# Kernel tuning notes

Measured on AMD Instinct MI355X. Metric: run time of the kernel, lower is better.

Reference implementation:

```python
import jax, jax.numpy as jnp
import numpy as np

# Structural constants (derived from anchors_list in the original forward)
NUM_PER_LEVEL = [98304, 49152, 24576, 12288, 6144]
NUM_ANCHORS_PER_LOC = 3
CAND_PER_LEVEL = 9  # candidate_number_of_positive_anchors_per_level
SMOOTH_L1_NA = 3.0  # self.num_anchors -> smooth-L1 beta = 1/3
INF = 100000000.0


def _build_anchors():
    parts = []
    for lvl, n in enumerate(NUM_PER_LEVEL):
        locs = n // NUM_ANCHORS_PER_LOC
        stride = 8.0 * (2 ** lvl)
        centers = (np.arange(locs) + 0.5) * stride
        base = 16.0 * (2 ** lvl)
        widths = base * np.array([1.0, 2 ** (1.0 / 3.0), 2 ** (2.0 / 3.0)])
        c = np.repeat(centers, NUM_ANCHORS_PER_LOC)
        w = np.tile(widths, locs)
        parts.append(np.stack([c - w / 2.0, c + w / 2.0], axis=1))
    return np.concatenate(parts, axis=0).astype(np.float32)


def setup_inputs() -> dict:
    key = jax.random.key(0)
    k1, k2, k3 = jax.random.split(key, 3)
    anchors = jnp.asarray(_build_anchors())  # [A, 2]
    A = anchors.shape[0]
    B, M = 4, 64
    extent = (NUM_PER_LEVEL[0] // NUM_ANCHORS_PER_LOC) * 8.0
    centers = jax.random.uniform(k1, (B, M), minval=0.0, maxval=extent)
    widths = jax.random.uniform(k2, (B, M), minval=50.0, maxval=500.0)
    # class column = 0, class_id = 1 -> every GT row survives the filter
    annotations = jnp.stack(
        [centers - widths / 2.0, centers + widths / 2.0, jnp.zeros((B, M))], axis=-1
    ).astype(jnp.float32)
    regressions = jax.random.normal(k3, (B, A, 2), dtype=jnp.float32)
    return {"regressions": regressions, "anchors": anchors,
            "annotations": annotations, "class_id": 1}


def _calc_iou_1d(a, b):
    # a: [A,2] anchors, b: [M,2] gt intervals -> IoU [A, M]
    inter = jnp.clip(
        jnp.minimum(a[:, 1][:, None], b[:, 1][None, :])
        - jnp.maximum(a[:, 0][:, None], b[:, 0][None, :]), 0.0)
    union = (a[:, 1] - a[:, 0])[:, None] + (b[:, 1] - b[:, 0])[None, :] - inter
    return inter / jnp.clip(union, 1e-8)


def _atss_l1_loss_single(regression, annotation, anchors):
    A = anchors.shape[0]
    M = annotation.shape[0]
    iou = _calc_iou_1d(anchors, annotation[:, :2])  # [A, M]

    anchor_cx = (anchors[:, 0] + anchors[:, 1]) / 2.0
    gt_cx = (annotation[:, 0] + annotation[:, 1]) / 2.0
    # gt_y and anchor_y are both 0 -> Euclidean distance reduces to |dx|
    dist = jnp.abs(anchor_cx[:, None] - gt_cx[None, :])  # [A, M]

    # per-level topk (smallest distance) candidates
    cand_idx_list = []
    start = 0
    for n in NUM_PER_LEVEL:
        topk = min(CAND_PER_LEVEL * NUM_ANCHORS_PER_LOC, n)
        _, idx = jax.lax.top_k(-dist[start:start + n].T, topk)  # [M, topk]
        cand_idx_list.append(idx.T + start)
        start += n
    cand_idx = jnp.concatenate(cand_idx_list, axis=0)  # [K, M], K = 27*levels
    K = cand_idx.shape[0]

    cand_iou = jnp.take_along_axis(iou, cand_idx, axis=0)  # [K, M]
    iou_mean = cand_iou.mean(axis=0)
    iou_std = jnp.sqrt(jnp.sum((cand_iou - iou_mean[None, :]) ** 2, axis=0)
                       / (K - 1))  # unbiased, like torch.std
    thresh = iou_mean + iou_std
    is_pos = cand_iou >= thresh[None, :]

    # candidate center must be inside the gt interval (margin 0.01)
    cand_cx = anchor_cx[cand_idx]  # [K, M]
    l = cand_cx - annotation[None, :, 0]
    r = annotation[None, :, 1] - cand_cx
    is_pos = is_pos & (jnp.minimum(l, r) > 0.01)

    # scatter candidate IoUs into [M*A] buffer of -INF, then per-anchor argmax over gts
    flat_idx = (cand_idx + jnp.arange(M)[None, :] * A).ravel()  # unique indices
    iou_t_flat = iou.T.ravel()
    vals = jnp.where(is_pos.ravel(), iou_t_flat[flat_idx], -INF)
    ious_inf = jnp.full((M * A,), -INF, dtype=iou.dtype).at[flat_idx].set(vals)
    ious_inf = ious_inf.reshape(M, A).T  # [A, M]

    best_val = ious_inf.max(axis=1)
    best_idx = jnp.argmax(ious_inf, axis=1)
    pos = best_val != -INF  # [A]

    assigned = annotation[best_idx]  # [A, 3]
    anchor_w = anchors[:, 1] - anchors[:, 0]
    anchor_c = anchors[:, 0] + 0.5 * anchor_w
    gt_w_raw = assigned[:, 1] - assigned[:, 0]
    gt_c = assigned[:, 0] + 0.5 * gt_w_raw  # center uses unclamped width
    gt_w = jnp.clip(gt_w_raw, 1.0)

    dx = (gt_c - anchor_c) / anchor_w / 0.1
    dw = jnp.log(gt_w / anchor_w) / 0.2
    targets = jnp.stack([dx, dw], axis=-1)  # [A, 2]

    diff = jnp.abs(targets - regression)
    beta = 1.0 / SMOOTH_L1_NA
    loss = jnp.where(diff <= beta,
                     0.5 * SMOOTH_L1_NA * diff ** 2,
                     diff - 0.5 / SMOOTH_L1_NA)
    mask = pos.astype(loss.dtype)[:, None]
    num_pos = jnp.sum(pos)
    loss_mean = jnp.sum(loss * mask) / jnp.maximum(num_pos * 2, 1).astype(loss.dtype)
    return jnp.where(num_pos > 0, loss_mean, jnp.zeros((), loss.dtype))


def reference(regressions, anchors, annotations, class_id):
    # class_id only drives the GT filter; inputs are built so all rows are kept
    # (class column != -1 and != class_id).
    per_image = jax.vmap(lambda r, a: _atss_l1_loss_single(r, a, anchors))
    return per_image(regressions, annotations)  # [B] per-image losses
```

## Files before the change

### kernel.cpp

```cpp
#include <hip/hip_runtime.h>


static constexpr int NLEV = 5;
static constexpr int B_IMG = 4;
static constexpr int M_GT = 64;
static constexpr int A_TOTAL = 190464;
static constexpr int K_CAND = 135;
static constexpr int BM_TOTAL = B_IMG * M_GT;
static constexpr int REC_STRIDE = 136;
static constexpr int SLICES = 16;
static constexpr int MAX_J = 9;
static constexpr unsigned long long PACK_BIAS = 0xB000000000000000ULL;

__device__ __constant__ int d_LOCS[NLEV]   = {32768, 16384, 8192, 4096, 2048};
__device__ __constant__ int d_ASTART[NLEV] = {0, 98304, 147456, 172032, 184320};

__global__ __launch_bounds__(64) void atss_assign(
    const float* __restrict__ reg,
    const float* __restrict__ anchors,
    const float* __restrict__ ann,
    unsigned long long* __restrict__ packed,
    unsigned long long* __restrict__ rec)
{
    const int bm = blockIdx.x;
    const int b = bm >> 6;
    const int m = bm & 63;
    const int lane = threadIdx.x;

    const float g0 = ann[(b * M_GT + m) * 3 + 0];
    const float g1 = ann[(b * M_GT + m) * 3 + 1];
    const float gcx = (g0 + g1) * 0.5f;

    int   j_[NLEV];
    float a0v[NLEV], a1v[NLEV];
#pragma unroll
    for (int lvl = 0; lvl < NLEV; ++lvl) {
        const int locs = d_LOCS[lvl];
        const int base = d_ASTART[lvl];
        const float stride = (float)(8 << lvl);
        int j = (int)(gcx / stride);
        if (j < 0) j = 0;
        if (j > locs - 1) j = locs - 1;
        j_[lvl] = j;
        const int t = j - 10 + lane;
        const bool v = (lane < 21) && (t >= 0) && (t < locs);
        const int a = base + 3 * t;
        a0v[lvl] = v ? anchors[2 * a]     : 0.0f;
        a1v[lvl] = v ? anchors[2 * a + 1] : 0.0f;
    }

    int winStart[NLEV];
#pragma unroll
    for (int lvl = 0; lvl < NLEV; ++lvl) {
        const int locs = d_LOCS[lvl];
        const int j = j_[lvl];
        const int t = j - 10 + lane;
        const bool v = (lane < 21) && (t >= 0) && (t < locs);
        const float dist =
            v ? fabsf((a0v[lvl] + a1v[lvl]) * 0.5f - gcx) : INFINITY;

        int bi = 10;
        float bd = INFINITY;
#pragma unroll
        for (int li = 9; li <= 11; ++li) {
            const float d = __shfl(dist, li);
            if (d < bd) { bd = d; bi = li; }
        }

        int lo = bi, hi = bi;
#pragma unroll
        for (int s = 0; s < 8; ++s) {
            const float dl = __shfl(dist, lo - 1);
            const float dr = __shfl(dist, hi + 1);
            if (dl <= dr) --lo; else ++hi;
        }
        winStart[lvl] = (j - 10) + lo;
    }

    float ci[3];
    int   ca[3];
    bool  cok[3];
    float ca0[3], ca1[3];
#pragma unroll
    for (int i = 0; i < 3; ++i) {
        const int k = lane + 64 * i;
        ci[i] = 0.0f; ca[i] = -1; cok[i] = false; ca0[i] = 0.0f; ca1[i] = 1.0f;
        if (k < K_CAND) {
            const int lvl = k / 27;
            const int r = k % 27;
            const int loc = winStart[lvl] + r / 3;
            const int a = d_ASTART[lvl] + loc * 3 + (r % 3);
            const float a0 = anchors[2 * a];
            const float a1 = anchors[2 * a + 1];
            float inter = fminf(a1, g1) - fmaxf(a0, g0);
            inter = fmaxf(inter, 0.0f);
            const float uni = (a1 - a0) + (g1 - g0) - inter;
            const float iou = inter / fmaxf(uni, 1e-8f);
            const float cx = (a0 + a1) * 0.5f;
            ci[i] = iou;
            ca[i] = a;
            ca0[i] = a0;
            ca1[i] = a1;
            cok[i] = fminf(cx - g0, g1 - cx) > 0.01f;
        }
    }

    float r0[3], r1[3];
#pragma unroll
    for (int i = 0; i < 3; ++i) {
        r0[i] = 0.0f; r1[i] = 0.0f;
        if (ca[i] >= 0) {
            const float* r = reg + ((size_t)b * A_TOTAL + ca[i]) * 2;
            r0[i] = r[0];
            r1[i] = r[1];
        }
    }

    float s = ci[0] + ci[1] + ci[2];
#pragma unroll
    for (int off = 32; off >= 1; off >>= 1) s += __shfl_xor(s, off);
    const float mean = s / 135.0f;

    float s2 = 0.0f;
#pragma unroll
    for (int i = 0; i < 3; ++i) {
        if (ca[i] >= 0) { const float d = ci[i] - mean; s2 += d * d; }
    }
#pragma unroll
    for (int off = 32; off >= 1; off >>= 1) s2 += __shfl_xor(s2, off);
    const float thresh = mean + sqrtf(s2 / 134.0f);

    unsigned long long* pb = packed + (size_t)b * A_TOTAL;
    bool pos[3];
#pragma unroll
    for (int i = 0; i < 3; ++i) {
        pos[i] = (ca[i] >= 0) && cok[i] && (ci[i] >= thresh);
        if (pos[i]) {
            const unsigned long long pk =
                (((unsigned long long)__float_as_uint(ci[i]) << 32) |
                 (unsigned int)(~m)) + PACK_BIAS;
            atomicMax(pb + ca[i], pk);
        }
    }

    const float gwr = g1 - g0;
    const float gc = g0 + 0.5f * gwr;
    const float gw = fmaxf(gwr, 1.0f);
    float lossv[3];
#pragma unroll
    for (int i = 0; i < 3; ++i) {
        lossv[i] = 0.0f;
        if (pos[i]) {
            const float a0 = ca0[i];
            const float a1 = ca1[i];
            const float aw = a1 - a0;
            const float acx = a0 + 0.5f * aw;
            const float dx = (gc - acx) / aw / 0.1f;
            const float dw = logf(gw / aw) / 0.2f;
            const float d0 = fabsf(dx - r0[i]);
            const float d1 = fabsf(dw - r1[i]);
            const float beta = 1.0f / 3.0f;
            const float l0 = (d0 <= beta) ? 0.5f * 3.0f * d0 * d0 : d0 - 0.5f / 3.0f;
            const float l1 = (d1 <= beta) ? 0.5f * 3.0f * d1 * d1 : d1 - 0.5f / 3.0f;
            lossv[i] = l0 + l1;
        }
    }

    const unsigned long long m0 = __ballot(pos[0]);
    const unsigned long long m1 = __ballot(pos[1]);
    const unsigned long long m2 = __ballot(pos[2]);
    const int c0 = __popcll(m0);
    const int c1 = __popcll(m1);
    const unsigned long long below63 =
        (lane == 63) ? 0x7FFFFFFFFFFFFFFFULL : ((1ULL << lane) - 1ULL);
    const int base = bm * REC_STRIDE;
    int offs[3];
    offs[0] = __popcll(m0 & below63);
    offs[1] = c0 + __popcll(m1 & below63);
    offs[2] = c0 + c1 + __popcll(m2 & below63);
#pragma unroll
    for (int i = 0; i < 3; ++i) {
        if (pos[i]) {
            rec[base + offs[i]] =
                ((unsigned long long)__float_as_uint(lossv[i]) << 32) |
                ((unsigned long long)(unsigned int)m << 18) |
                (unsigned int)ca[i];
        }
    }
    if (lane == 0) {
        rec[base + (REC_STRIDE - 1)] =
            (unsigned long long)(c0 + c1 + __popcll(m2));
    }
}

__global__ __launch_bounds__(1024) void atss_resolve(
    const unsigned long long* __restrict__ packed,
    const unsigned long long* __restrict__ rec,
    float* __restrict__ out)
{
    const int b = blockIdx.x;
    const int tid = threadIdx.x;
    const int gt = tid >> 4;
    const int slice = tid & 15;
    const int wave = tid >> 6;
    const int lane = tid & 63;

    const int region = b * M_GT + gt;
    const int base = region * REC_STRIDE;
    const unsigned long long* pb = packed + (size_t)b * A_TOTAL;

    const unsigned long long cv = rec[base + (REC_STRIDE - 1)];
    unsigned long long al[MAX_J];
#pragma unroll
    for (int j = 0; j < MAX_J; ++j) {
        al[j] = rec[base + slice + SLICES * j];
    }

    unsigned int c = (unsigned int)cv;
    if (c > (unsigned int)K_CAND) c = K_CAND;

    unsigned long long cur[MAX_J];
#pragma unroll
    for (int j = 0; j < MAX_J; ++j) {
        const bool valid = (unsigned int)(slice + SLICES * j) < c;
        const unsigned int a = (unsigned int)al[j] & 0x3FFFFu;
        cur[j] = valid
            ? __hip_atomic_load(pb + a, __ATOMIC_RELAXED,
                                __HIP_MEMORY_SCOPE_AGENT)
            : 0ULL;
    }

    float L = 0.0f, C = 0.0f;
#pragma unroll
    for (int j = 0; j < MAX_J; ++j) {
        if ((unsigned int)(slice + SLICES * j) < c) {
            const unsigned int mr = ((unsigned int)al[j] >> 18) & 63u;
            if ((unsigned int)cur[j] == ~mr) {
                L += __uint_as_float((unsigned int)(al[j] >> 32));
                C += 1.0f;
            }
        }
    }

#pragma unroll
    for (int off = 32; off >= 1; off >>= 1) {
        L += __shfl_xor(L, off);
        C += __shfl_xor(C, off);
    }

    __shared__ float sl[16];
    __shared__ float sc[16];
    if (lane == 0) { sl[wave] = L; sc[wave] = C; }
    __syncthreads();

    if (tid == 0) {
        float Lt = 0.0f, Ct = 0.0f;
#pragma unroll
        for (int w = 0; w < 16; ++w) { Lt += sl[w]; Ct += sc[w]; }
        const unsigned int np = (unsigned int)Ct;
        const unsigned int denom = (2u * np > 1u) ? 2u * np : 1u;
        out[b] = (np > 0) ? Lt / (float)denom : 0.0f;
    }
}

extern "C" void kernel_launch(void* const* d_in, const int* in_sizes, int n_in,
                              void* d_out, int out_size, void* d_ws, size_t ws_size,
                              hipStream_t stream) {
    const float* reg     = (const float*)d_in[0];
    const float* anchors = (const float*)d_in[1];
    const float* ann     = (const float*)d_in[2];
    float* out = (float*)d_out;

    char* p = (char*)d_ws;
    unsigned long long* packed = (unsigned long long*)p;
    p += (size_t)B_IMG * A_TOTAL * 8;
    unsigned long long* rec = (unsigned long long*)p;

    atss_assign<<<BM_TOTAL, 64, 0, stream>>>(reg, anchors, ann, packed, rec);
    atss_resolve<<<B_IMG, 1024, 0, stream>>>(packed, rec, out);
}
```

Baseline: 15.53 us.

## Fuse assign and resolve kernels into one launch with flag-based inter-block sync

Merges the per-GT assignment kernel and the per-image resolve kernel into a single launch. Sixteen producer blocks of 16 waves each replace the 256 single-wave blocks, and publish their records with agent-scope atomic stores plus a release flag per GT. Four consumer blocks spin on those flags with sleep before reading. This removes the second kernel launch and its dependency gap. In exchange it relies on all blocks being co-resident, and on the flag region not holding magic values left over from an earlier call.

```diff
diff --git a/kernel.cpp b/kernel.cpp
--- a/kernel.cpp
+++ b/kernel.cpp
@@ -10,196 +10,214 @@
 static constexpr int REC_STRIDE = 136;
 static constexpr int SLICES = 16;
 static constexpr int MAX_J = 9;
+static constexpr int PROD_BLOCKS = 16;
 static constexpr unsigned long long PACK_BIAS = 0xB000000000000000ULL;
+static constexpr unsigned long long FLAG_MAGIC = 0x5AFEC0DEF00D0000ULL;
 
 __device__ __constant__ int d_LOCS[NLEV]   = {32768, 16384, 8192, 4096, 2048};
 __device__ __constant__ int d_ASTART[NLEV] = {0, 98304, 147456, 172032, 184320};
 
-__global__ __launch_bounds__(64) void atss_assign(
+__global__ __launch_bounds__(1024) void atss_fused(
     const float* __restrict__ reg,
     const float* __restrict__ anchors,
     const float* __restrict__ ann,
     unsigned long long* __restrict__ packed,
-    unsigned long long* __restrict__ rec)
-{
-    const int bm = blockIdx.x;
-    const int b = bm >> 6;
-    const int m = bm & 63;
-    const int lane = threadIdx.x;
-
-    const float g0 = ann[(b * M_GT + m) * 3 + 0];
-    const float g1 = ann[(b * M_GT + m) * 3 + 1];
-    const float gcx = (g0 + g1) * 0.5f;
-
-    int   j_[NLEV];
-    float a0v[NLEV], a1v[NLEV];
-#pragma unroll
-    for (int lvl = 0; lvl < NLEV; ++lvl) {
-        const int locs = d_LOCS[lvl];
-        const int base = d_ASTART[lvl];
-        const float stride = (float)(8 << lvl);
-        int j = (int)(gcx / stride);
-        if (j < 0) j = 0;
-        if (j > locs - 1) j = locs - 1;
-        j_[lvl] = j;
-        const int t = j - 10 + lane;
-        const bool v = (lane < 21) && (t >= 0) && (t < locs);
-        const int a = base + 3 * t;
-        a0v[lvl] = v ? anchors[2 * a]     : 0.0f;
-        a1v[lvl] = v ? anchors[2 * a + 1] : 0.0f;
-    }
-
-    int winStart[NLEV];
-#pragma unroll
-    for (int lvl = 0; lvl < NLEV; ++lvl) {
-        const int locs = d_LOCS[lvl];
-        const int j = j_[lvl];
-        const int t = j - 10 + lane;
-        const bool v = (lane < 21) && (t >= 0) && (t < locs);
-        const float dist =
-            v ? fabsf((a0v[lvl] + a1v[lvl]) * 0.5f - gcx) : INFINITY;
-
-        int bi = 10;
-        float bd = INFINITY;
-#pragma unroll
-        for (int li = 9; li <= 11; ++li) {
-            const float d = __shfl(dist, li);
-            if (d < bd) { bd = d; bi = li; }
-        }
-
-        int lo = bi, hi = bi;
-#pragma unroll
-        for (int s = 0; s < 8; ++s) {
-            const float dl = __shfl(dist, lo - 1);
-            const float dr = __shfl(dist, hi + 1);
-            if (dl <= dr) --lo; else ++hi;
-        }
-        winStart[lvl] = (j - 10) + lo;
-    }
-
-    float ci[3];
-    int   ca[3];
-    bool  cok[3];
-    float ca0[3], ca1[3];
-#pragma unroll
-    for (int i = 0; i < 3; ++i) {
-        const int k = lane + 64 * i;
-        ci[i] = 0.0f; ca[i] = -1; cok[i] = false; ca0[i] = 0.0f; ca1[i] = 1.0f;
-        if (k < K_CAND) {
-            const int lvl = k / 27;
-            const int r = k % 27;
-            const int loc = winStart[lvl] + r / 3;
-            const int a = d_ASTART[lvl] + loc * 3 + (r % 3);
-            const float a0 = anchors[2 * a];
-            const float a1 = anchors[2 * a + 1];
-            float inter = fminf(a1, g1) - fmaxf(a0, g0);
-            inter = fmaxf(inter, 0.0f);
-            const float uni = (a1 - a0) + (g1 - g0) - inter;
-            const float iou = inter / fmaxf(uni, 1e-8f);
-            const float cx = (a0 + a1) * 0.5f;
-            ci[i] = iou;
-            ca[i] = a;
-            ca0[i] = a0;
-            ca1[i] = a1;
-            cok[i] = fminf(cx - g0, g1 - cx) > 0.01f;
-        }
-    }
-
-    float r0[3], r1[3];
-#pragma unroll
-    for (int i = 0; i < 3; ++i) {
-        r0[i] = 0.0f; r1[i] = 0.0f;
-        if (ca[i] >= 0) {
-            const float* r = reg + ((size_t)b * A_TOTAL + ca[i]) * 2;
-            r0[i] = r[0];
-            r1[i] = r[1];
-        }
-    }
-
-    float s = ci[0] + ci[1] + ci[2];
-#pragma unroll
-    for (int off = 32; off >= 1; off >>= 1) s += __shfl_xor(s, off);
-    const float mean = s / 135.0f;
-
-    float s2 = 0.0f;
-#pragma unroll
-    for (int i = 0; i < 3; ++i) {
-        if (ca[i] >= 0) { const float d = ci[i] - mean; s2 += d * d; }
-    }
-#pragma unroll
-    for (int off = 32; off >= 1; off >>= 1) s2 += __shfl_xor(s2, off);
-    const float thresh = mean + sqrtf(s2 / 134.0f);
-
-    unsigned long long* pb = packed + (size_t)b * A_TOTAL;
-    bool pos[3];
-#pragma unroll
-    for (int i = 0; i < 3; ++i) {
-        pos[i] = (ca[i] >= 0) && cok[i] && (ci[i] >= thresh);
-        if (pos[i]) {
-            const unsigned long long pk =
-                (((unsigned long long)__float_as_uint(ci[i]) << 32) |
-                 (unsigned int)(~m)) + PACK_BIAS;
-            atomicMax(pb + ca[i], pk);
-        }
-    }
-
-    const float gwr = g1 - g0;
-    const float gc = g0 + 0.5f * gwr;
-    const float gw = fmaxf(gwr, 1.0f);
-    float lossv[3];
-#pragma unroll
-    for (int i = 0; i < 3; ++i) {
-        lossv[i] = 0.0f;
-        if (pos[i]) {
-            const float a0 = ca0[i];
-            const float a1 = ca1[i];
-            const float aw = a1 - a0;
-            const float acx = a0 + 0.5f * aw;
-            const float dx = (gc - acx) / aw / 0.1f;
-            const float dw = logf(gw / aw) / 0.2f;
-            const float d0 = fabsf(dx - r0[i]);
-            const float d1 = fabsf(dw - r1[i]);
-            const float beta = 1.0f / 3.0f;
-            const float l0 = (d0 <= beta) ? 0.5f * 3.0f * d0 * d0 : d0 - 0.5f / 3.0f;
-            const float l1 = (d1 <= beta) ? 0.5f * 3.0f * d1 * d1 : d1 - 0.5f / 3.0f;
-            lossv[i] = l0 + l1;
-        }
-    }
-
-    const unsigned long long m0 = __ballot(pos[0]);
-    const unsigned long long m1 = __ballot(pos[1]);
-    const unsigned long long m2 = __ballot(pos[2]);
-    const int c0 = __popcll(m0);
-    const int c1 = __popcll(m1);
-    const unsigned long long below63 =
-        (lane == 63) ? 0x7FFFFFFFFFFFFFFFULL : ((1ULL << lane) - 1ULL);
-    const int base = bm * REC_STRIDE;
-    int offs[3];
-    offs[0] = __popcll(m0 & below63);
-    offs[1] = c0 + __popcll(m1 & below63);
-    offs[2] = c0 + c1 + __popcll(m2 & below63);
-#pragma unroll
-    for (int i = 0; i < 3; ++i) {
-        if (pos[i]) {
-            rec[base + offs[i]] =
-                ((unsigned long long)__float_as_uint(lossv[i]) << 32) |
-                ((unsigned long long)(unsigned int)m << 18) |
-                (unsigned int)ca[i];
-        }
-    }
-    if (lane == 0) {
-        rec[base + (REC_STRIDE - 1)] =
-            (unsigned long long)(c0 + c1 + __popcll(m2));
-    }
-}
-
-__global__ __launch_bounds__(1024) void atss_resolve(
-    const unsigned long long* __restrict__ packed,
-    const unsigned long long* __restrict__ rec,
+    unsigned long long* __restrict__ rec,
+    unsigned long long* __restrict__ flag,
     float* __restrict__ out)
 {
-    const int b = blockIdx.x;
+    const int blk = blockIdx.x;
     const int tid = threadIdx.x;
+
+    if (blk < PROD_BLOCKS) {
+        const int wave = tid >> 6;
+        const int lane = tid & 63;
+        const int bm = blk * 16 + wave;
+        const int b = bm >> 6;
+        const int m = bm & 63;
+
+        const float g0 = ann[(b * M_GT + m) * 3 + 0];
+        const float g1 = ann[(b * M_GT + m) * 3 + 1];
+        const float gcx = (g0 + g1) * 0.5f;
+
+        int   j_[NLEV];
+        float a0v[NLEV], a1v[NLEV];
+#pragma unroll
+        for (int lvl = 0; lvl < NLEV; ++lvl) {
+            const int locs = d_LOCS[lvl];
+            const int base = d_ASTART[lvl];
+            const float stride = (float)(8 << lvl);
+            int j = (int)(gcx / stride);
+            if (j < 0) j = 0;
+            if (j > locs - 1) j = locs - 1;
+            j_[lvl] = j;
+            const int t = j - 10 + lane;
+            const bool v = (lane < 21) && (t >= 0) && (t < locs);
+            const int a = base + 3 * t;
+            a0v[lvl] = v ? anchors[2 * a]     : 0.0f;
+            a1v[lvl] = v ? anchors[2 * a + 1] : 0.0f;
+        }
+
+        int winStart[NLEV];
+#pragma unroll
+        for (int lvl = 0; lvl < NLEV; ++lvl) {
+            const int locs = d_LOCS[lvl];
+            const int j = j_[lvl];
+            const int t = j - 10 + lane;
+            const bool v = (lane < 21) && (t >= 0) && (t < locs);
+            const float dist =
+                v ? fabsf((a0v[lvl] + a1v[lvl]) * 0.5f - gcx) : INFINITY;
+
+            int bi = 10;
+            float bd = INFINITY;
+#pragma unroll
+            for (int li = 9; li <= 11; ++li) {
+                const float d = __shfl(dist, li, 64);
+                if (d < bd) { bd = d; bi = li; }
+            }
+
+            int lo = bi, hi = bi;
+#pragma unroll
+            for (int s = 0; s < 8; ++s) {
+                const float dl = __shfl(dist, lo - 1, 64);
+                const float dr = __shfl(dist, hi + 1, 64);
+                if (dl <= dr) --lo; else ++hi;
+            }
+            winStart[lvl] = (j - 10) + lo;
+        }
+
+        float ci[3];
+        int   ca[3];
+        bool  cok[3];
+        float ca0[3], ca1[3];
+#pragma unroll
+        for (int i = 0; i < 3; ++i) {
+            const int k = lane + 64 * i;
+            ci[i] = 0.0f; ca[i] = -1; cok[i] = false;
+            ca0[i] = 0.0f; ca1[i] = 1.0f;
+            if (k < K_CAND) {
+                const int lvl = k / 27;
+                const int r = k % 27;
+                const int loc = winStart[lvl] + r / 3;
+                const int a = d_ASTART[lvl] + loc * 3 + (r % 3);
+                const float a0 = anchors[2 * a];
+                const float a1 = anchors[2 * a + 1];
+                float inter = fminf(a1, g1) - fmaxf(a0, g0);
+                inter = fmaxf(inter, 0.0f);
+                const float uni = (a1 - a0) + (g1 - g0) - inter;
+                const float iou = inter / fmaxf(uni, 1e-8f);
+                const float cx = (a0 + a1) * 0.5f;
+                ci[i] = iou;
+                ca[i] = a;
+                ca0[i] = a0;
+                ca1[i] = a1;
+                cok[i] = fminf(cx - g0, g1 - cx) > 0.01f;
+            }
+        }
+
+        float r0[3], r1[3];
+#pragma unroll
+        for (int i = 0; i < 3; ++i) {
+            r0[i] = 0.0f; r1[i] = 0.0f;
+            if (ca[i] >= 0) {
+                const float* r = reg + ((size_t)b * A_TOTAL + ca[i]) * 2;
+                r0[i] = r[0];
+                r1[i] = r[1];
+            }
+        }
+
+        float s = ci[0] + ci[1] + ci[2];
+#pragma unroll
+        for (int off = 32; off >= 1; off >>= 1) s += __shfl_xor(s, off, 64);
+        const float mean = s / 135.0f;
+
+        float s2 = 0.0f;
+#pragma unroll
+        for (int i = 0; i < 3; ++i) {
+            if (ca[i] >= 0) { const float d = ci[i] - mean; s2 += d * d; }
+        }
+#pragma unroll
+        for (int off = 32; off >= 1; off >>= 1) s2 += __shfl_xor(s2, off, 64);
+        const float thresh = mean + sqrtf(s2 / 134.0f);
+
+        unsigned long long* pb = packed + (size_t)b * A_TOTAL;
+        bool pos[3];
+#pragma unroll
+        for (int i = 0; i < 3; ++i) {
+            pos[i] = (ca[i] >= 0) && cok[i] && (ci[i] >= thresh);
+            if (pos[i]) {
+                const unsigned long long pk =
+                    (((unsigned long long)__float_as_uint(ci[i]) << 32) |
+                     (unsigned int)(~m)) + PACK_BIAS;
+                atomicMax(pb + ca[i], pk);
+            }
+        }
+
+        const float gwr = g1 - g0;
+        const float gc = g0 + 0.5f * gwr;
+        const float gw = fmaxf(gwr, 1.0f);
+        float lossv[3];
+#pragma unroll
+        for (int i = 0; i < 3; ++i) {
+            lossv[i] = 0.0f;
+            if (pos[i]) {
+                const float a0 = ca0[i];
+                const float a1 = ca1[i];
+                const float aw = a1 - a0;
+                const float acx = a0 + 0.5f * aw;
+                const float dx = (gc - acx) / aw / 0.1f;
+                const float dw = logf(gw / aw) / 0.2f;
+                const float d0 = fabsf(dx - r0[i]);
+                const float d1 = fabsf(dw - r1[i]);
+                const float beta = 1.0f / 3.0f;
+                const float l0 = (d0 <= beta) ? 0.5f * 3.0f * d0 * d0
+                                              : d0 - 0.5f / 3.0f;
+                const float l1 = (d1 <= beta) ? 0.5f * 3.0f * d1 * d1
+                                              : d1 - 0.5f / 3.0f;
+                lossv[i] = l0 + l1;
+            }
+        }
+
+        const unsigned long long m0 = __ballot(pos[0]);
+        const unsigned long long m1 = __ballot(pos[1]);
+        const unsigned long long m2 = __ballot(pos[2]);
+        const int c0 = __popcll(m0);
+        const int c1 = __popcll(m1);
+        const unsigned long long below63 =
+            (lane == 63) ? 0x7FFFFFFFFFFFFFFFULL : ((1ULL << lane) - 1ULL);
+        const int base = bm * REC_STRIDE;
+        int offs[3];
+        offs[0] = __popcll(m0 & below63);
+        offs[1] = c0 + __popcll(m1 & below63);
+        offs[2] = c0 + c1 + __popcll(m2 & below63);
+#pragma unroll
+        for (int i = 0; i < 3; ++i) {
+            if (pos[i]) {
+                const unsigned long long r64 =
+                    ((unsigned long long)__float_as_uint(lossv[i]) << 32) |
+                    ((unsigned long long)(unsigned int)m << 18) |
+                    (unsigned int)ca[i];
+                __hip_atomic_store(rec + base + offs[i], r64,
+                                   __ATOMIC_RELAXED,
+                                   __HIP_MEMORY_SCOPE_AGENT);
+            }
+        }
+        if (lane == 0) {
+            __hip_atomic_store(rec + base + (REC_STRIDE - 1),
+                               (unsigned long long)(c0 + c1 + __popcll(m2)),
+                               __ATOMIC_RELAXED, __HIP_MEMORY_SCOPE_AGENT);
+        }
+
+        __threadfence();
+        if (lane == 0) {
+            __hip_atomic_store(flag + bm,
+                               FLAG_MAGIC + (unsigned long long)bm,
+                               __ATOMIC_RELEASE, __HIP_MEMORY_SCOPE_AGENT);
+        }
+        return;
+    }
+
+    const int b = blk - PROD_BLOCKS;
     const int gt = tid >> 4;
     const int slice = tid & 15;
     const int wave = tid >> 6;
@@ -209,15 +227,28 @@
     const int base = region * REC_STRIDE;
     const unsigned long long* pb = packed + (size_t)b * A_TOTAL;
 
-    const unsigned long long cv = rec[base + (REC_STRIDE - 1)];
+    const unsigned long long expect =
+        FLAG_MAGIC + (unsigned long long)region;
+    while (__hip_atomic_load(flag + region, __ATOMIC_ACQUIRE,
+                             __HIP_MEMORY_SCOPE_AGENT) != expect) {
+        __builtin_amdgcn_s_sleep(2);
+    }
+
+    const unsigned long long cv = __hip_atomic_load(
+        rec + base + (REC_STRIDE - 1), __ATOMIC_RELAXED,
+        __HIP_MEMORY_SCOPE_AGENT);
     unsigned long long al[MAX_J];
 #pragma unroll
     for (int j = 0; j < MAX_J; ++j) {
-        al[j] = rec[base + slice + SLICES * j];
+        al[j] = __hip_atomic_load(rec + base + slice + SLICES * j,
+                                  __ATOMIC_RELAXED,
+                                  __HIP_MEMORY_SCOPE_AGENT);
     }
 
     unsigned int c = (unsigned int)cv;
     if (c > (unsigned int)K_CAND) c = K_CAND;
+
+    __syncthreads();
 
     unsigned long long cur[MAX_J];
 #pragma unroll
@@ -244,8 +275,8 @@
 
 #pragma unroll
     for (int off = 32; off >= 1; off >>= 1) {
-        L += __shfl_xor(L, off);
-        C += __shfl_xor(C, off);
+        L += __shfl_xor(L, off, 64);
+        C += __shfl_xor(C, off, 64);
     }
 
     __shared__ float sl[16];
@@ -275,7 +306,9 @@
     unsigned long long* packed = (unsigned long long*)p;
     p += (size_t)B_IMG * A_TOTAL * 8;
     unsigned long long* rec = (unsigned long long*)p;
-
-    atss_assign<<<BM_TOTAL, 64, 0, stream>>>(reg, anchors, ann, packed, rec);
-    atss_resolve<<<B_IMG, 1024, 0, stream>>>(packed, rec, out);
+    p += ((size_t)BM_TOTAL * REC_STRIDE + 16) * 8;
+    unsigned long long* flag = (unsigned long long*)p;
+
+    atss_fused<<<PROD_BLOCKS + B_IMG, 1024, 0, stream>>>(
+        reg, anchors, ann, packed, rec, flag, out);
 }
```

Measured after the change: 25.07 us. +61.4%, slower.
